# Kernel optimization log

Hardware: AMD Instinct MI355X
Metric: run time of the kernel (lower is better)

## Reference

```python
import jax, jax.numpy as jnp
import numpy as np

SIN, TEMB, EMB, S = 128, 512, 1024, 64
BATCH, T = 4, 4096


def setup_inputs() -> dict:
    key = jax.random.key(0)
    ks = jax.random.split(key, 16)

    def w(k, *shape):
        return jax.random.normal(k, shape, jnp.float32) / np.float32(np.sqrt(shape[0]))

    return {
        "time_embed": jax.random.normal(ks[0], (SIN,), jnp.float32),
        "x": jax.random.normal(ks[1], (BATCH, T, EMB), jnp.float32),
        "W1": w(ks[2], SIN, TEMB), "b1": jnp.zeros((TEMB,), jnp.float32),
        "W2": w(ks[3], TEMB, TEMB), "b2": jnp.zeros((TEMB,), jnp.float32),
        "WA": w(ks[4], TEMB, S), "bA": jnp.zeros((S,), jnp.float32),
        "WB": w(ks[5], TEMB, S, EMB), "bB": jnp.zeros((S, EMB), jnp.float32),
        "WC": w(ks[6], TEMB, EMB, S), "bC": jnp.zeros((EMB, S), jnp.float32),
        "WD": w(ks[7], TEMB, EMB), "bD": jnp.zeros((EMB,), jnp.float32),
        "Wdl": w(ks[8], TEMB, S), "bdl": jnp.zeros((S,), jnp.float32),
        "MA": w(ks[9], SIN, S), "mA": jnp.zeros((S,), jnp.float32),
        "MB": w(ks[10], SIN, S, EMB), "mB": jnp.zeros((S, EMB), jnp.float32),
        "MC": w(ks[11], SIN, EMB, S), "mC": jnp.zeros((EMB, S), jnp.float32),
        "MD": w(ks[12], SIN, EMB), "mD": jnp.zeros((EMB,), jnp.float32),
        "Mdl": w(ks[13], SIN, S), "mdl": jnp.zeros((S,), jnp.float32),
    }


def _ssm_forward(time_embed, x, W1, b1, W2, b2, WA, bA, WB, bB, WC, bC, WD, bD,
                 Wdl, bdl, MA, mA, MB, mB, MC, mC, MD, mD, Mdl, mdl):
    # time-dependent parameter generation
    t = jax.nn.silu(time_embed @ W1 + b1)
    t = t @ W2 + b2  # [TEMB]

    A_base = -jax.nn.softplus(t @ WA + bA)                       # [S]
    B_base = jnp.einsum('t,tse->se', t, WB) + bB                 # [S,E]
    C_base = jnp.einsum('t,tes->es', t, WC) + bC                 # [E,S]
    D_base = t @ WD + bD                                         # [E]
    delta_base = jax.nn.softplus(t @ Wdl + bdl) + 1e-4           # [S]

    A = A_base * jax.nn.sigmoid(time_embed @ MA + mA)
    Bm = B_base * jax.nn.sigmoid(jnp.einsum('t,tse->se', time_embed, MB) + mB)
    C = C_base * jax.nn.sigmoid(jnp.einsum('t,tes->es', time_embed, MC) + mC)
    D = D_base * jax.nn.sigmoid(time_embed @ MD + mD)
    delta = delta_base * jax.nn.sigmoid(time_embed @ Mdl + mdl)  # [S]

    A_bar = jnp.exp(delta * A)          # [S]
    B_bar = delta[:, None] * Bm         # [S,E]

    xt = jnp.swapaxes(x, 0, 1)          # [T,B,E]

    def step(h, x_t):                   # h: [B,S], x_t: [B,E]
        h_new = A_bar * h + x_t @ B_bar.T
        y = h_new @ C.T                 # [B,E]
        return h_new, y

    h0 = jnp.zeros((x.shape[0], A_bar.shape[0]), x.dtype)
    _, ys = jax.lax.scan(step, h0, xt)  # ys: [T,B,E]
    return jnp.swapaxes(ys, 0, 1) + D * x


def reference(time_embed, x, W1, b1, W2, b2, WA, bA, WB, bB, WC, bC, WD, bD,
              Wdl, bdl, MA, mA, MB, mB, MC, mC, MD, mD, Mdl, mdl):
    return _ssm_forward(time_embed, x, W1, b1, W2, b2, WA, bA, WB, bB, WC, bC,
                        WD, bD, Wdl, bdl, MA, mA, MB, mB, MC, mC, MD, mD, Mdl, mdl)
```

## Files before the change

kernel.cpp:

```cpp
#include <hip/hip_runtime.h>
#include <math.h>

#define SIN_ 128
#define TEMB_ 512
#define EMB_ 1024
#define S_ 64
#define B_ 4
#define T_ 4096
#define NROW (B_*T_)
#define L_ 64
#define NC_ (T_/L_)

#define PSTR 132224
#define FA   132096
#define FDL  132160

#define WS_T1     0
#define WS_T2     512
#define WS_DELTA  1024
#define WS_ABAR   1088
#define WS_EL     1152
#define WS_FAC    1216
#define WS_D      5312
#define WS_BMT    6336
#define WS_CT     71872
#define WS_P      137408
#define WS_HLOC   798528
#define WS_CHEND  1847104
#define WS_CARRY  1863488

__device__ __forceinline__ float sigmoidf_(float x){ return 1.f/(1.f+expf(-x)); }
__device__ __forceinline__ float softplusf_(float x){ return x>20.f ? x : log1pf(expf(x)); }
__device__ __forceinline__ float4 sig4_(float4 g){
  float4 r; r.x=sigmoidf_(g.x); r.y=sigmoidf_(g.y); r.z=sigmoidf_(g.z); r.w=sigmoidf_(g.w); return r;
}

__global__ void k_t1(const float* __restrict__ te, const float* __restrict__ W1,
                     const float* __restrict__ b1, float* __restrict__ ws){
  __shared__ float ste[SIN_];
  int tid = threadIdx.x;
  ste[tid] = te[tid]; ste[tid+64] = te[tid+64];
  __syncthreads();
  int j = blockIdx.x*64 + tid;
  float a = b1[j];
  #pragma unroll 16
  for (int i=0;i<SIN_;i++) a += ste[i]*W1[i*TEMB_ + j];
  ws[WS_T1 + j] = a * sigmoidf_(a);
}

__global__ __launch_bounds__(512) void k_t2(const float* __restrict__ W2,
                                            const float* __restrict__ b2,
                                            float* __restrict__ ws){
  __shared__ float st1[TEMB_];
  __shared__ float red[8][64];
  int tid = threadIdx.x;
  st1[tid] = ws[WS_T1 + tid];
  __syncthreads();
  int jl = tid & 63, kc = tid >> 6;
  int j = blockIdx.x*64 + jl;
  float p = 0.f;
  #pragma unroll 8
  for (int i=0;i<64;i++){
    int k = kc*64 + i;
    p += st1[k]*W2[k*TEMB_ + j];
  }
  red[kc][jl] = p;
  __syncthreads();
  if (tid < 64){
    float a = b2[blockIdx.x*64 + tid];
    #pragma unroll
    for (int c=0;c<8;c++) a += red[c][tid];
    ws[WS_T2 + blockIdx.x*64 + tid] = a;
  }
}

__global__ __launch_bounds__(256) void k_partial(
    const float* __restrict__ te,
    const float* __restrict__ WB, const float* __restrict__ MB,
    const float* __restrict__ WC, const float* __restrict__ MC,
    const float* __restrict__ WD, const float* __restrict__ MD,
    const float* __restrict__ WA, const float* __restrict__ MA,
    const float* __restrict__ Wdl, const float* __restrict__ Mdl,
    float* __restrict__ ws){
  __shared__ float st2[TEMB_];
  __shared__ float ste[SIN_];
  int tid = threadIdx.x;
  st2[tid] = ws[WS_T2 + tid];
  st2[tid+256] = ws[WS_T2 + tid + 256];
  if (tid < SIN_) ste[tid] = te[tid];
  __syncthreads();
  int bb = blockIdx.x;
  if (bb < 640){
    int region = bb < 320 ? 0 : 1;
    int lb = bb - region*320;
    int tile = lb/5, ch = lb - tile*5;
    int q = tile*256 + tid;
    float4 a = {0.f,0.f,0.f,0.f};
    if (ch < 4){
      const float4* W4 = (const float4*)(region==0 ? WB : WC) + (size_t)(ch*128)*16384 + q;
      const float* coef = st2 + ch*128;
      #pragma unroll 8
      for (int i=0;i<128;i++){
        float4 w = W4[(size_t)i*16384];
        float c = coef[i];
        a.x += c*w.x; a.y += c*w.y; a.z += c*w.z; a.w += c*w.w;
      }
    } else {
      const float4* W4 = (const float4*)(region==0 ? MB : MC) + q;
      #pragma unroll 8
      for (int i=0;i<128;i++){
        float4 w = W4[(size_t)i*16384];
        float c = ste[i];
        a.x += c*w.x; a.y += c*w.y; a.z += c*w.z; a.w += c*w.w;
      }
    }
    ((float4*)(ws + WS_P + ch*PSTR))[region*16384 + q] = a;
  } else if (bb < 645){
    int ch = bb - 640;
    float4 a = {0.f,0.f,0.f,0.f};
    if (ch < 4){
      const float4* W4 = (const float4*)WD + (ch*128)*256 + tid;
      const float* coef = st2 + ch*128;
      #pragma unroll 8
      for (int i=0;i<128;i++){
        float4 w = W4[i*256];
        float c = coef[i];
        a.x += c*w.x; a.y += c*w.y; a.z += c*w.z; a.w += c*w.w;
      }
    } else {
      const float4* W4 = (const float4*)MD + tid;
      #pragma unroll 8
      for (int i=0;i<128;i++){
        float4 w = W4[i*256];
        float c = ste[i];
        a.x += c*w.x; a.y += c*w.y; a.z += c*w.z; a.w += c*w.w;
      }
    }
    ((float4*)(ws + WS_P + ch*PSTR))[32768 + tid] = a;
  } else if (bb == 645){
    int c = tid>>6, s = tid&63;
    float p = 0.f;
    #pragma unroll 8
    for (int i=0;i<128;i++) p += st2[c*128+i]*WA[(c*128+i)*64 + s];
    ws[WS_P + c*PSTR + FA + s] = p;
    if (tid < 64){
      float g = 0.f;
      #pragma unroll 8
      for (int i=0;i<128;i++) g += ste[i]*MA[i*64 + s];
      ws[WS_P + 4*PSTR + FA + s] = g;
    }
  } else {
    int c = tid>>6, s = tid&63;
    float p = 0.f;
    #pragma unroll 8
    for (int i=0;i<128;i++) p += st2[c*128+i]*Wdl[(c*128+i)*64 + s];
    ws[WS_P + c*PSTR + FDL + s] = p;
    if (tid < 64){
      float g = 0.f;
      #pragma unroll 8
      for (int i=0;i<128;i++) g += ste[i]*Mdl[i*64 + s];
      ws[WS_P + 4*PSTR + FDL + s] = g;
    }
  }
}

__global__ __launch_bounds__(256) void k_finalize(
    const float* __restrict__ bB, const float* __restrict__ mB,
    const float* __restrict__ bC, const float* __restrict__ mC,
    const float* __restrict__ bD, const float* __restrict__ mD,
    const float* __restrict__ bA_, const float* __restrict__ mA_,
    const float* __restrict__ bdl, const float* __restrict__ mdl,
    float* __restrict__ ws){
  int tid = threadIdx.x, bb = blockIdx.x;
  if (bb < 128){
    int q = bb*256 + tid;
    float4 a = ((const float4*)(ws + WS_P + 0*PSTR))[q];
    float4 a1 = ((const float4*)(ws + WS_P + 1*PSTR))[q];
    float4 a2 = ((const float4*)(ws + WS_P + 2*PSTR))[q];
    float4 a3 = ((const float4*)(ws + WS_P + 3*PSTR))[q];
    float4 g  = ((const float4*)(ws + WS_P + 4*PSTR))[q];
    a.x += a1.x+a2.x+a3.x; a.y += a1.y+a2.y+a3.y;
    a.z += a1.z+a2.z+a3.z; a.w += a1.w+a2.w+a3.w;
    if (q < 16384){
      float4 b4 = ((const float4*)bB)[q];
      float4 m4 = ((const float4*)mB)[q];
      float4 sg = sig4_(make_float4(g.x+m4.x, g.y+m4.y, g.z+m4.z, g.w+m4.w));
      float4 v = make_float4((a.x+b4.x)*sg.x,(a.y+b4.y)*sg.y,(a.z+b4.z)*sg.z,(a.w+b4.w)*sg.w);
      int o = q*4; int s = o>>10; int e = o&1023;
      ws[WS_BMT + (e+0)*64 + s] = v.x;
      ws[WS_BMT + (e+1)*64 + s] = v.y;
      ws[WS_BMT + (e+2)*64 + s] = v.z;
      ws[WS_BMT + (e+3)*64 + s] = v.w;
    } else {
      int q2 = q - 16384;
      float4 b4 = ((const float4*)bC)[q2];
      float4 m4 = ((const float4*)mC)[q2];
      float4 sg = sig4_(make_float4(g.x+m4.x, g.y+m4.y, g.z+m4.z, g.w+m4.w));
      float4 v = make_float4((a.x+b4.x)*sg.x,(a.y+b4.y)*sg.y,(a.z+b4.z)*sg.z,(a.w+b4.w)*sg.w);
      int o = q2*4; int e = o>>6; int s = o&63;
      ws[WS_CT + (s+0)*1024 + e] = v.x;
      ws[WS_CT + (s+1)*1024 + e] = v.y;
      ws[WS_CT + (s+2)*1024 + e] = v.z;
      ws[WS_CT + (s+3)*1024 + e] = v.w;
    }
  } else if (bb == 128){
    int q = 32768 + tid;
    float4 a = ((const float4*)(ws + WS_P + 0*PSTR))[q];
    float4 a1 = ((const float4*)(ws + WS_P + 1*PSTR))[q];
    float4 a2 = ((const float4*)(ws + WS_P + 2*PSTR))[q];
    float4 a3 = ((const float4*)(ws + WS_P + 3*PSTR))[q];
    float4 g  = ((const float4*)(ws + WS_P + 4*PSTR))[q];
    a.x += a1.x+a2.x+a3.x; a.y += a1.y+a2.y+a3.y;
    a.z += a1.z+a2.z+a3.z; a.w += a1.w+a2.w+a3.w;
    float4 b4 = ((const float4*)bD)[tid];
    float4 m4 = ((const float4*)mD)[tid];
    float4 sg = sig4_(make_float4(g.x+m4.x, g.y+m4.y, g.z+m4.z, g.w+m4.w));
    float4 v = make_float4((a.x+b4.x)*sg.x,(a.y+b4.y)*sg.y,(a.z+b4.z)*sg.z,(a.w+b4.w)*sg.w);
    ((float4*)(ws + WS_D))[tid] = v;
  } else {
    __shared__ float sda[64];
    if (tid < 64){
      int s = tid;
      float sa = ws[WS_P+0*PSTR+FA+s]+ws[WS_P+1*PSTR+FA+s]+ws[WS_P+2*PSTR+FA+s]+ws[WS_P+3*PSTR+FA+s];
      float ga = ws[WS_P+4*PSTR+FA+s];
      float A = -softplusf_(sa + bA_[s]) * sigmoidf_(ga + mA_[s]);
      float sd = ws[WS_P+0*PSTR+FDL+s]+ws[WS_P+1*PSTR+FDL+s]+ws[WS_P+2*PSTR+FDL+s]+ws[WS_P+3*PSTR+FDL+s];
      float gd = ws[WS_P+4*PSTR+FDL+s];
      float delta = (softplusf_(sd + bdl[s]) + 1e-4f) * sigmoidf_(gd + mdl[s]);
      float da = delta * A;
      sda[s] = da;
      ws[WS_DELTA+s] = delta;
      ws[WS_ABAR+s]  = expf(da);
      ws[WS_EL+s]    = expf(64.f*da);
    }
    __syncthreads();
    for (int idx=tid; idx<L_*S_; idx+=256){
      int tl = idx>>6, s = idx&63;
      ws[WS_FAC+idx] = expf((float)(tl+1)*sda[s]);
    }
  }
}

__global__ __launch_bounds__(256) void k_scan(const float* __restrict__ x, float* __restrict__ ws){
  __shared__ float Xs[64][68];
  __shared__ float BsT[64][68];
  __shared__ float Us[64][65];
  __shared__ float sdl[S_], sab[S_];
  int tid = threadIdx.x;
  int bb = blockIdx.x;
  int row0 = (bb>>6)*T_ + (bb&63)*64;
  if (tid<64){ sdl[tid]=ws[WS_DELTA+tid]; sab[tid]=ws[WS_ABAR+tid]; }
  float acc[4][4];
  #pragma unroll
  for (int i=0;i<4;i++)
    #pragma unroll
    for (int j=0;j<4;j++) acc[i][j]=0.f;
  int ty = tid>>4, tx = tid&15;
  const float4* x4 = (const float4*)x;
  const float4* BmT4 = (const float4*)(ws + WS_BMT);
  for (int kk=0; kk<EMB_; kk+=64){
    #pragma unroll
    for (int t=0;t<4;t++){
      int fl = t*256+tid; int rr = fl>>4, cq = fl&15;
      float4 xv = x4[(size_t)(row0+rr)*256 + (kk>>2) + cq];
      *(float4*)&Xs[rr][cq*4] = xv;
      float4 bv = BmT4[(size_t)(kk+rr)*16 + cq];
      *(float4*)&BsT[rr][cq*4] = bv;
    }
    __syncthreads();
    #pragma unroll 8
    for (int k=0;k<64;k++){
      float4 b4 = *(const float4*)&BsT[k][4*tx];
      float x0 = Xs[4*ty+0][k], x1 = Xs[4*ty+1][k], x2 = Xs[4*ty+2][k], x3 = Xs[4*ty+3][k];
      acc[0][0]+=x0*b4.x; acc[0][1]+=x0*b4.y; acc[0][2]+=x0*b4.z; acc[0][3]+=x0*b4.w;
      acc[1][0]+=x1*b4.x; acc[1][1]+=x1*b4.y; acc[1][2]+=x1*b4.z; acc[1][3]+=x1*b4.w;
      acc[2][0]+=x2*b4.x; acc[2][1]+=x2*b4.y; acc[2][2]+=x2*b4.z; acc[2][3]+=x2*b4.w;
      acc[3][0]+=x3*b4.x; acc[3][1]+=x3*b4.y; acc[3][2]+=x3*b4.z; acc[3][3]+=x3*b4.w;
    }
    __syncthreads();
  }
  #pragma unroll
  for (int i=0;i<4;i++)
    #pragma unroll
    for (int j=0;j<4;j++)
      Us[4*ty+i][4*tx+j] = acc[i][j]*sdl[4*tx+j];
  __syncthreads();
  if (tid<64){
    int s = tid; float h = 0.f, ab = sab[s];
    for (int t=0;t<64;t++){
      h = fmaf(ab, h, Us[t][s]);
      ws[WS_HLOC + (row0+t)*S_ + s] = h;
    }
    ws[WS_CHEND + bb*S_ + s] = h;
  }
}

__global__ void k_carry(float* __restrict__ ws){
  __shared__ float ch[B_*NC_*S_];
  int tid = threadIdx.x;
  for (int i=tid;i<B_*NC_*S_;i+=256) ch[i] = ws[WS_CHEND + i];
  __syncthreads();
  int b = tid>>6, s = tid&63;
  float el = ws[WS_EL + s];
  float carry = 0.f;
  #pragma unroll 8
  for (int c=0;c<NC_;c++){
    int idx = (b*NC_ + c)*S_ + s;
    ws[WS_CARRY + idx] = carry;
    carry = el*carry + ch[idx];
  }
}

__global__ __launch_bounds__(256) void k_out(const float* __restrict__ x,
                                             const float* __restrict__ ws,
                                             float* __restrict__ out){
  __shared__ float Cts[64][68];
  __shared__ float Hs[64][68];
  int tid = threadIdx.x;
  int bb = blockIdx.x;
  int rt = bb & 255, et = bb >> 8;
  int row0 = rt*64, e0 = et*64;
  int b = row0 >> 12;
  int cidx = (row0 & (T_-1)) >> 6;
  int cbase4 = ((b*NC_ + cidx)*S_) >> 2;
  const float4* hl4 = (const float4*)(ws + WS_HLOC);
  const float4* fc4 = (const float4*)(ws + WS_FAC);
  const float4* cr4 = (const float4*)(ws + WS_CARRY);
  const float4* CT4 = (const float4*)(ws + WS_CT);
  #pragma unroll
  for (int t=0;t<4;t++){
    int fl = t*256+tid; int rr = fl>>4, q = fl&15;
    float4 h = hl4[(size_t)(row0+rr)*16 + q];
    float4 f = fc4[rr*16 + q];
    float4 c = cr4[cbase4 + q];
    float4 hv = make_float4(h.x+f.x*c.x, h.y+f.y*c.y, h.z+f.z*c.z, h.w+f.w*c.w);
    *(float4*)&Hs[rr][q*4] = hv;
    float4 ct = CT4[(size_t)rr*256 + (e0>>2) + q];
    *(float4*)&Cts[rr][q*4] = ct;
  }
  __syncthreads();
  int ty = tid>>4, tx = tid&15;
  float acc[4][4];
  #pragma unroll
  for (int i=0;i<4;i++)
    #pragma unroll
    for (int j=0;j<4;j++) acc[i][j]=0.f;
  #pragma unroll 8
  for (int s=0;s<64;s++){
    float4 c4 = *(const float4*)&Cts[s][4*tx];
    float h0 = Hs[4*ty+0][s], h1 = Hs[4*ty+1][s], h2 = Hs[4*ty+2][s], h3 = Hs[4*ty+3][s];
    acc[0][0]+=h0*c4.x; acc[0][1]+=h0*c4.y; acc[0][2]+=h0*c4.z; acc[0][3]+=h0*c4.w;
    acc[1][0]+=h1*c4.x; acc[1][1]+=h1*c4.y; acc[1][2]+=h1*c4.z; acc[1][3]+=h1*c4.w;
    acc[2][0]+=h2*c4.x; acc[2][1]+=h2*c4.y; acc[2][2]+=h2*c4.z; acc[2][3]+=h2*c4.w;
    acc[3][0]+=h3*c4.x; acc[3][1]+=h3*c4.y; acc[3][2]+=h3*c4.z; acc[3][3]+=h3*c4.w;
  }
  float4 d4 = ((const float4*)(ws + WS_D))[(e0>>2) + tx];
  #pragma unroll
  for (int i=0;i<4;i++){
    int row = row0 + 4*ty + i;
    float4 x4v = reinterpret_cast<const float4*>(x + (size_t)row*EMB_ + e0)[tx];
    float4 o;
    o.x = acc[i][0] + d4.x*x4v.x;
    o.y = acc[i][1] + d4.y*x4v.y;
    o.z = acc[i][2] + d4.z*x4v.z;
    o.w = acc[i][3] + d4.w*x4v.w;
    reinterpret_cast<float4*>(out + (size_t)row*EMB_ + e0)[tx] = o;
  }
}

extern "C" void kernel_launch(void* const* d_in, const int* in_sizes, int n_in,
                              void* d_out, int out_size, void* d_ws, size_t ws_size,
                              hipStream_t stream){
  const float* te  = (const float*)d_in[0];
  const float* x   = (const float*)d_in[1];
  const float* W1  = (const float*)d_in[2];
  const float* b1  = (const float*)d_in[3];
  const float* W2  = (const float*)d_in[4];
  const float* b2  = (const float*)d_in[5];
  const float* WA  = (const float*)d_in[6];
  const float* bA  = (const float*)d_in[7];
  const float* WB  = (const float*)d_in[8];
  const float* bB  = (const float*)d_in[9];
  const float* WC  = (const float*)d_in[10];
  const float* bC  = (const float*)d_in[11];
  const float* WD  = (const float*)d_in[12];
  const float* bD  = (const float*)d_in[13];
  const float* Wdl = (const float*)d_in[14];
  const float* bdl = (const float*)d_in[15];
  const float* MA  = (const float*)d_in[16];
  const float* mA  = (const float*)d_in[17];
  const float* MB  = (const float*)d_in[18];
  const float* mB  = (const float*)d_in[19];
  const float* MC  = (const float*)d_in[20];
  const float* mC  = (const float*)d_in[21];
  const float* MD  = (const float*)d_in[22];
  const float* mD  = (const float*)d_in[23];
  const float* Mdl = (const float*)d_in[24];
  const float* mdl = (const float*)d_in[25];
  float* ws  = (float*)d_ws;
  float* out = (float*)d_out;

  k_t1<<<8,64,0,stream>>>(te, W1, b1, ws);
  k_t2<<<8,512,0,stream>>>(W2, b2, ws);
  k_partial<<<647,256,0,stream>>>(te, WB,MB, WC,MC, WD,MD, WA,MA, Wdl,Mdl, ws);
  k_finalize<<<130,256,0,stream>>>(bB,mB, bC,mC, bD,mD, bA,mA, bdl,mdl, ws);
  k_scan<<<256,256,0,stream>>>(x, ws);
  k_carry<<<1,256,0,stream>>>(ws);
  k_out<<<4096,256,0,stream>>>(x, ws, out);
}
```

Measured before the change: 185.3 us.

## Halve scan chunk length and split weight reductions into finer chunks with prefetch

Cuts the scan chunk length from 64 to 32 timesteps, doubling the k_scan grid to 512 blocks and shortening the serial per-chunk recurrence. k_partial splits each K-reduction into ten 64-row chunks (1292 blocks) and uses a software-prefetched colsum helper to raise memory-level parallelism on the large WB/WC/MB/MC weight reads. k_finalize sums the extra partials, and k_carry reads chunk ends directly from global memory instead of staging them in shared memory. The workspace is re-laid out so HLOC overlaps the partial buffer. In exchange, the serial k_carry loop gets twice as many chunks and k_scan re-reads Bm once per 32 rows instead of per 64.

```diff
diff --git a/kernel.cpp b/kernel.cpp
--- a/kernel.cpp
+++ b/kernel.cpp
@@ -8,7 +8,7 @@
 #define B_ 4
 #define T_ 4096
 #define NROW (B_*T_)
-#define L_ 64
+#define L_ 32
 #define NC_ (T_/L_)
 
 #define PSTR 132224
@@ -21,18 +21,46 @@
 #define WS_ABAR   1088
 #define WS_EL     1152
 #define WS_FAC    1216
-#define WS_D      5312
-#define WS_BMT    6336
-#define WS_CT     71872
-#define WS_P      137408
-#define WS_HLOC   798528
-#define WS_CHEND  1847104
-#define WS_CARRY  1863488
+#define WS_D      3264
+#define WS_BMT    4288
+#define WS_CT     69824
+#define WS_P      135360
+#define WS_HLOC   135360
+#define WS_CHEND  1183936
+#define WS_CARRY  1216704
 
 __device__ __forceinline__ float sigmoidf_(float x){ return 1.f/(1.f+expf(-x)); }
 __device__ __forceinline__ float softplusf_(float x){ return x>20.f ? x : log1pf(expf(x)); }
 __device__ __forceinline__ float4 sig4_(float4 g){
   float4 r; r.x=sigmoidf_(g.x); r.y=sigmoidf_(g.y); r.z=sigmoidf_(g.z); r.w=sigmoidf_(g.w); return r;
+}
+
+__device__ __forceinline__ float4 colsum64(const float4* __restrict__ W, size_t strideB,
+                                           const float* __restrict__ coef){
+  const char* p = (const char*)W;
+  float4 b0 = *(const float4*)p;
+  float4 b1 = *(const float4*)(p + strideB);
+  float4 b2 = *(const float4*)(p + 2*strideB);
+  float4 b3 = *(const float4*)(p + 3*strideB);
+  p += 4*strideB;
+  float4 acc = {0.f,0.f,0.f,0.f};
+  #pragma unroll
+  for (int step=0; step<16; ++step){
+    float4 c0v=b0, c1v=b1, c2v=b2, c3v=b3;
+    if (step < 15){
+      b0 = *(const float4*)p;
+      b1 = *(const float4*)(p + strideB);
+      b2 = *(const float4*)(p + 2*strideB);
+      b3 = *(const float4*)(p + 3*strideB);
+      p += 4*strideB;
+    }
+    float c0 = coef[4*step+0], c1 = coef[4*step+1], c2 = coef[4*step+2], c3 = coef[4*step+3];
+    acc.x = fmaf(c0,c0v.x,acc.x); acc.y = fmaf(c0,c0v.y,acc.y); acc.z = fmaf(c0,c0v.z,acc.z); acc.w = fmaf(c0,c0v.w,acc.w);
+    acc.x = fmaf(c1,c1v.x,acc.x); acc.y = fmaf(c1,c1v.y,acc.y); acc.z = fmaf(c1,c1v.z,acc.z); acc.w = fmaf(c1,c1v.w,acc.w);
+    acc.x = fmaf(c2,c2v.x,acc.x); acc.y = fmaf(c2,c2v.y,acc.y); acc.z = fmaf(c2,c2v.z,acc.z); acc.w = fmaf(c2,c2v.w,acc.w);
+    acc.x = fmaf(c3,c3v.x,acc.x); acc.y = fmaf(c3,c3v.y,acc.y); acc.z = fmaf(c3,c3v.z,acc.z); acc.w = fmaf(c3,c3v.w,acc.w);
+  }
+  return acc;
 }
 
 __global__ void k_t1(const float* __restrict__ te, const float* __restrict__ W1,
@@ -90,54 +118,36 @@
   if (tid < SIN_) ste[tid] = te[tid];
   __syncthreads();
   int bb = blockIdx.x;
-  if (bb < 640){
-    int region = bb < 320 ? 0 : 1;
-    int lb = bb - region*320;
-    int tile = lb/5, ch = lb - tile*5;
+  if (bb < 1280){
+    int region = bb >= 640 ? 1 : 0;
+    int lb = bb - region*640;
+    int tile = lb/10, ch = lb - tile*10;
     int q = tile*256 + tid;
-    float4 a = {0.f,0.f,0.f,0.f};
-    if (ch < 4){
-      const float4* W4 = (const float4*)(region==0 ? WB : WC) + (size_t)(ch*128)*16384 + q;
-      const float* coef = st2 + ch*128;
-      #pragma unroll 8
-      for (int i=0;i<128;i++){
-        float4 w = W4[(size_t)i*16384];
-        float c = coef[i];
-        a.x += c*w.x; a.y += c*w.y; a.z += c*w.z; a.w += c*w.w;
-      }
+    const float4* base;
+    const float* coef;
+    if (ch < 8){
+      base = (const float4*)(region==0 ? WB : WC) + (size_t)(ch*64)*16384 + q;
+      coef = st2 + ch*64;
     } else {
-      const float4* W4 = (const float4*)(region==0 ? MB : MC) + q;
-      #pragma unroll 8
-      for (int i=0;i<128;i++){
-        float4 w = W4[(size_t)i*16384];
-        float c = ste[i];
-        a.x += c*w.x; a.y += c*w.y; a.z += c*w.z; a.w += c*w.w;
-      }
-    }
+      base = (const float4*)(region==0 ? MB : MC) + (size_t)((ch-8)*64)*16384 + q;
+      coef = ste + (ch-8)*64;
+    }
+    float4 a = colsum64(base, (size_t)16384*16, coef);
     ((float4*)(ws + WS_P + ch*PSTR))[region*16384 + q] = a;
-  } else if (bb < 645){
-    int ch = bb - 640;
-    float4 a = {0.f,0.f,0.f,0.f};
-    if (ch < 4){
-      const float4* W4 = (const float4*)WD + (ch*128)*256 + tid;
-      const float* coef = st2 + ch*128;
-      #pragma unroll 8
-      for (int i=0;i<128;i++){
-        float4 w = W4[i*256];
-        float c = coef[i];
-        a.x += c*w.x; a.y += c*w.y; a.z += c*w.z; a.w += c*w.w;
-      }
+  } else if (bb < 1290){
+    int ch = bb - 1280;
+    const float4* base;
+    const float* coef;
+    if (ch < 8){
+      base = (const float4*)WD + (ch*64)*256 + tid;
+      coef = st2 + ch*64;
     } else {
-      const float4* W4 = (const float4*)MD + tid;
-      #pragma unroll 8
-      for (int i=0;i<128;i++){
-        float4 w = W4[i*256];
-        float c = ste[i];
-        a.x += c*w.x; a.y += c*w.y; a.z += c*w.z; a.w += c*w.w;
-      }
-    }
+      base = (const float4*)MD + ((ch-8)*64)*256 + tid;
+      coef = ste + (ch-8)*64;
+    }
+    float4 a = colsum64(base, (size_t)256*16, coef);
     ((float4*)(ws + WS_P + ch*PSTR))[32768 + tid] = a;
-  } else if (bb == 645){
+  } else if (bb == 1290){
     int c = tid>>6, s = tid&63;
     float p = 0.f;
     #pragma unroll 8
@@ -172,51 +182,47 @@
     const float* __restrict__ bdl, const float* __restrict__ mdl,
     float* __restrict__ ws){
   int tid = threadIdx.x, bb = blockIdx.x;
-  if (bb < 128){
-    int q = bb*256 + tid;
-    float4 a = ((const float4*)(ws + WS_P + 0*PSTR))[q];
-    float4 a1 = ((const float4*)(ws + WS_P + 1*PSTR))[q];
-    float4 a2 = ((const float4*)(ws + WS_P + 2*PSTR))[q];
-    float4 a3 = ((const float4*)(ws + WS_P + 3*PSTR))[q];
-    float4 g  = ((const float4*)(ws + WS_P + 4*PSTR))[q];
-    a.x += a1.x+a2.x+a3.x; a.y += a1.y+a2.y+a3.y;
-    a.z += a1.z+a2.z+a3.z; a.w += a1.w+a2.w+a3.w;
-    if (q < 16384){
-      float4 b4 = ((const float4*)bB)[q];
-      float4 m4 = ((const float4*)mB)[q];
+  if (bb < 129){
+    int q = (bb < 128) ? bb*256 + tid : 32768 + tid;
+    float4 a = {0.f,0.f,0.f,0.f};
+    #pragma unroll
+    for (int c=0;c<8;c++){
+      float4 v = ((const float4*)(ws + WS_P + c*PSTR))[q];
+      a.x += v.x; a.y += v.y; a.z += v.z; a.w += v.w;
+    }
+    float4 g8 = ((const float4*)(ws + WS_P + 8*PSTR))[q];
+    float4 g9 = ((const float4*)(ws + WS_P + 9*PSTR))[q];
+    float4 g = make_float4(g8.x+g9.x, g8.y+g9.y, g8.z+g9.z, g8.w+g9.w);
+    if (bb < 128){
+      if (q < 16384){
+        float4 b4 = ((const float4*)bB)[q];
+        float4 m4 = ((const float4*)mB)[q];
+        float4 sg = sig4_(make_float4(g.x+m4.x, g.y+m4.y, g.z+m4.z, g.w+m4.w));
+        float4 v = make_float4((a.x+b4.x)*sg.x,(a.y+b4.y)*sg.y,(a.z+b4.z)*sg.z,(a.w+b4.w)*sg.w);
+        int o = q*4; int s = o>>10; int e = o&1023;
+        ws[WS_BMT + (e+0)*64 + s] = v.x;
+        ws[WS_BMT + (e+1)*64 + s] = v.y;
+        ws[WS_BMT + (e+2)*64 + s] = v.z;
+        ws[WS_BMT + (e+3)*64 + s] = v.w;
+      } else {
+        int q2 = q - 16384;
+        float4 b4 = ((const float4*)bC)[q2];
+        float4 m4 = ((const float4*)mC)[q2];
+        float4 sg = sig4_(make_float4(g.x+m4.x, g.y+m4.y, g.z+m4.z, g.w+m4.w));
+        float4 v = make_float4((a.x+b4.x)*sg.x,(a.y+b4.y)*sg.y,(a.z+b4.z)*sg.z,(a.w+b4.w)*sg.w);
+        int o = q2*4; int e = o>>6; int s = o&63;
+        ws[WS_CT + (s+0)*1024 + e] = v.x;
+        ws[WS_CT + (s+1)*1024 + e] = v.y;
+        ws[WS_CT + (s+2)*1024 + e] = v.z;
+        ws[WS_CT + (s+3)*1024 + e] = v.w;
+      }
+    } else {
+      float4 b4 = ((const float4*)bD)[tid];
+      float4 m4 = ((const float4*)mD)[tid];
       float4 sg = sig4_(make_float4(g.x+m4.x, g.y+m4.y, g.z+m4.z, g.w+m4.w));
       float4 v = make_float4((a.x+b4.x)*sg.x,(a.y+b4.y)*sg.y,(a.z+b4.z)*sg.z,(a.w+b4.w)*sg.w);
-      int o = q*4; int s = o>>10; int e = o&1023;
-      ws[WS_BMT + (e+0)*64 + s] = v.x;
-      ws[WS_BMT + (e+1)*64 + s] = v.y;
-      ws[WS_BMT + (e+2)*64 + s] = v.z;
-      ws[WS_BMT + (e+3)*64 + s] = v.w;
-    } else {
-      int q2 = q - 16384;
-      float4 b4 = ((const float4*)bC)[q2];
-      float4 m4 = ((const float4*)mC)[q2];
-      float4 sg = sig4_(make_float4(g.x+m4.x, g.y+m4.y, g.z+m4.z, g.w+m4.w));
-      float4 v = make_float4((a.x+b4.x)*sg.x,(a.y+b4.y)*sg.y,(a.z+b4.z)*sg.z,(a.w+b4.w)*sg.w);
-      int o = q2*4; int e = o>>6; int s = o&63;
-      ws[WS_CT + (s+0)*1024 + e] = v.x;
-      ws[WS_CT + (s+1)*1024 + e] = v.y;
-      ws[WS_CT + (s+2)*1024 + e] = v.z;
-      ws[WS_CT + (s+3)*1024 + e] = v.w;
-    }
-  } else if (bb == 128){
-    int q = 32768 + tid;
-    float4 a = ((const float4*)(ws + WS_P + 0*PSTR))[q];
-    float4 a1 = ((const float4*)(ws + WS_P + 1*PSTR))[q];
-    float4 a2 = ((const float4*)(ws + WS_P + 2*PSTR))[q];
-    float4 a3 = ((const float4*)(ws + WS_P + 3*PSTR))[q];
-    float4 g  = ((const float4*)(ws + WS_P + 4*PSTR))[q];
-    a.x += a1.x+a2.x+a3.x; a.y += a1.y+a2.y+a3.y;
-    a.z += a1.z+a2.z+a3.z; a.w += a1.w+a2.w+a3.w;
-    float4 b4 = ((const float4*)bD)[tid];
-    float4 m4 = ((const float4*)mD)[tid];
-    float4 sg = sig4_(make_float4(g.x+m4.x, g.y+m4.y, g.z+m4.z, g.w+m4.w));
-    float4 v = make_float4((a.x+b4.x)*sg.x,(a.y+b4.y)*sg.y,(a.z+b4.z)*sg.z,(a.w+b4.w)*sg.w);
-    ((float4*)(ws + WS_D))[tid] = v;
+      ((float4*)(ws + WS_D))[tid] = v;
+    }
   } else {
     __shared__ float sda[64];
     if (tid < 64){
@@ -231,7 +237,7 @@
       sda[s] = da;
       ws[WS_DELTA+s] = delta;
       ws[WS_ABAR+s]  = expf(da);
-      ws[WS_EL+s]    = expf(64.f*da);
+      ws[WS_EL+s]    = expf((float)L_*da);
     }
     __syncthreads();
     for (int idx=tid; idx<L_*S_; idx+=256){
@@ -242,17 +248,17 @@
 }
 
 __global__ __launch_bounds__(256) void k_scan(const float* __restrict__ x, float* __restrict__ ws){
-  __shared__ float Xs[64][68];
+  __shared__ float Xs[32][68];
   __shared__ float BsT[64][68];
-  __shared__ float Us[64][65];
+  __shared__ float Us[32][65];
   __shared__ float sdl[S_], sab[S_];
   int tid = threadIdx.x;
   int bb = blockIdx.x;
-  int row0 = (bb>>6)*T_ + (bb&63)*64;
+  int row0 = (bb>>7)*T_ + (bb&127)*L_;
   if (tid<64){ sdl[tid]=ws[WS_DELTA+tid]; sab[tid]=ws[WS_ABAR+tid]; }
-  float acc[4][4];
-  #pragma unroll
-  for (int i=0;i<4;i++)
+  float acc[2][4];
+  #pragma unroll
+  for (int i=0;i<2;i++)
     #pragma unroll
     for (int j=0;j<4;j++) acc[i][j]=0.f;
   int ty = tid>>4, tx = tid&15;
@@ -260,10 +266,14 @@
   const float4* BmT4 = (const float4*)(ws + WS_BMT);
   for (int kk=0; kk<EMB_; kk+=64){
     #pragma unroll
-    for (int t=0;t<4;t++){
+    for (int t=0;t<2;t++){
       int fl = t*256+tid; int rr = fl>>4, cq = fl&15;
       float4 xv = x4[(size_t)(row0+rr)*256 + (kk>>2) + cq];
       *(float4*)&Xs[rr][cq*4] = xv;
+    }
+    #pragma unroll
+    for (int t=0;t<4;t++){
+      int fl = t*256+tid; int rr = fl>>4, cq = fl&15;
       float4 bv = BmT4[(size_t)(kk+rr)*16 + cq];
       *(float4*)&BsT[rr][cq*4] = bv;
     }
@@ -271,23 +281,22 @@
     #pragma unroll 8
     for (int k=0;k<64;k++){
       float4 b4 = *(const float4*)&BsT[k][4*tx];
-      float x0 = Xs[4*ty+0][k], x1 = Xs[4*ty+1][k], x2 = Xs[4*ty+2][k], x3 = Xs[4*ty+3][k];
+      float x0 = Xs[2*ty+0][k], x1 = Xs[2*ty+1][k];
       acc[0][0]+=x0*b4.x; acc[0][1]+=x0*b4.y; acc[0][2]+=x0*b4.z; acc[0][3]+=x0*b4.w;
       acc[1][0]+=x1*b4.x; acc[1][1]+=x1*b4.y; acc[1][2]+=x1*b4.z; acc[1][3]+=x1*b4.w;
-      acc[2][0]+=x2*b4.x; acc[2][1]+=x2*b4.y; acc[2][2]+=x2*b4.z; acc[2][3]+=x2*b4.w;
-      acc[3][0]+=x3*b4.x; acc[3][1]+=x3*b4.y; acc[3][2]+=x3*b4.z; acc[3][3]+=x3*b4.w;
     }
     __syncthreads();
   }
   #pragma unroll
-  for (int i=0;i<4;i++)
+  for (int i=0;i<2;i++)
     #pragma unroll
     for (int j=0;j<4;j++)
-      Us[4*ty+i][4*tx+j] = acc[i][j]*sdl[4*tx+j];
+      Us[2*ty+i][4*tx+j] = acc[i][j]*sdl[4*tx+j];
   __syncthreads();
   if (tid<64){
     int s = tid; float h = 0.f, ab = sab[s];
-    for (int t=0;t<64;t++){
+    #pragma unroll 8
+    for (int t=0;t<L_;t++){
       h = fmaf(ab, h, Us[t][s]);
       ws[WS_HLOC + (row0+t)*S_ + s] = h;
     }
@@ -296,10 +305,7 @@
 }
 
 __global__ void k_carry(float* __restrict__ ws){
-  __shared__ float ch[B_*NC_*S_];
-  int tid = threadIdx.x;
-  for (int i=tid;i<B_*NC_*S_;i+=256) ch[i] = ws[WS_CHEND + i];
-  __syncthreads();
+  int tid = threadIdx.x;
   int b = tid>>6, s = tid&63;
   float el = ws[WS_EL + s];
   float carry = 0.f;
@@ -307,7 +313,7 @@
   for (int c=0;c<NC_;c++){
     int idx = (b*NC_ + c)*S_ + s;
     ws[WS_CARRY + idx] = carry;
-    carry = el*carry + ch[idx];
+    carry = fmaf(el, carry, ws[WS_CHEND + idx]);
   }
 }
 
@@ -321,8 +327,7 @@
   int rt = bb & 255, et = bb >> 8;
   int row0 = rt*64, e0 = et*64;
   int b = row0 >> 12;
-  int cidx = (row0 & (T_-1)) >> 6;
-  int cbase4 = ((b*NC_ + cidx)*S_) >> 2;
+  int cbase = b*NC_ + ((row0 & (T_-1)) >> 5);
   const float4* hl4 = (const float4*)(ws + WS_HLOC);
   const float4* fc4 = (const float4*)(ws + WS_FAC);
   const float4* cr4 = (const float4*)(ws + WS_CARRY);
@@ -331,8 +336,8 @@
   for (int t=0;t<4;t++){
     int fl = t*256+tid; int rr = fl>>4, q = fl&15;
     float4 h = hl4[(size_t)(row0+rr)*16 + q];
-    float4 f = fc4[rr*16 + q];
-    float4 c = cr4[cbase4 + q];
+    float4 f = fc4[(rr & (L_-1))*16 + q];
+    float4 c = cr4[(cbase + (rr>>5))*16 + q];
     float4 hv = make_float4(h.x+f.x*c.x, h.y+f.y*c.y, h.z+f.z*c.z, h.w+f.w*c.w);
     *(float4*)&Hs[rr][q*4] = hv;
     float4 ct = CT4[(size_t)rr*256 + (e0>>2) + q];
@@ -402,9 +407,9 @@
 
   k_t1<<<8,64,0,stream>>>(te, W1, b1, ws);
   k_t2<<<8,512,0,stream>>>(W2, b2, ws);
-  k_partial<<<647,256,0,stream>>>(te, WB,MB, WC,MC, WD,MD, WA,MA, Wdl,Mdl, ws);
+  k_partial<<<1292,256,0,stream>>>(te, WB,MB, WC,MC, WD,MD, WA,MA, Wdl,Mdl, ws);
   k_finalize<<<130,256,0,stream>>>(bB,mB, bC,mC, bD,mD, bA,mA, bdl,mdl, ws);
-  k_scan<<<256,256,0,stream>>>(x, ws);
+  k_scan<<<512,256,0,stream>>>(x, ws);
   k_carry<<<1,256,0,stream>>>(ws);
   k_out<<<4096,256,0,stream>>>(x, ws, out);
 }
```

Measured after the change: 197.5 us. +6.6%, slower.
